# Kernel optimization log

Hardware: AMD Instinct MI355X
Metric: run time of the kernel (lower is better)

## Reference

```python
import jax, jax.numpy as jnp
import numpy as np

NUM_HEADS = 32
NUM_KV_HEADS = 8
HEAD_DIM = 128
HIDDEN = 4096
ROPE_THETA = 10000.0
RMS_EPS = 1e-6


def setup_inputs() -> dict:
    key = jax.random.key(0)
    k1, k2, k3 = jax.random.split(key, 3)
    T = 2048
    qkv_out = (NUM_HEADS + 2 * NUM_KV_HEADS) * HEAD_DIM  # 6144
    return {
        "positions": jnp.arange(T, dtype=jnp.int64),
        "hidden_states": jax.random.normal(k1, (T, HIDDEN), dtype=jnp.float32),
        "wqkv": jax.random.normal(k2, (qkv_out, HIDDEN), dtype=jnp.float32) * 0.02,
        "wo": jax.random.normal(k3, (HIDDEN, NUM_HEADS * HEAD_DIM), dtype=jnp.float32) * 0.02,
        "q_norm_w": jnp.ones((HEAD_DIM,), dtype=jnp.float32),
        "k_norm_w": jnp.ones((HEAD_DIM,), dtype=jnp.float32),
    }


def _rms_norm(x, w):
    # per-head RMSNorm over last dim, computed in fp32 (matches Dots1RMSNorm)
    xf = x.astype(jnp.float32)
    var = jnp.mean(xf * xf, axis=-1, keepdims=True)
    return (w * (xf * jax.lax.rsqrt(var + RMS_EPS))).astype(x.dtype)


def _rope(x, positions):
    # NeoX-style rotary: rotate halves. x: [T, H, D]
    half = HEAD_DIM // 2
    inv_freq = 1.0 / (ROPE_THETA ** (jnp.arange(0, half, dtype=jnp.float32) / half))
    ang = positions.astype(jnp.float32)[:, None] * inv_freq  # [T, half]
    cos = jnp.cos(ang)[:, None, :]  # [T,1,half]
    sin = jnp.sin(ang)[:, None, :]
    x1, x2 = x[..., :half], x[..., half:]
    return jnp.concatenate([x1 * cos - x2 * sin, x2 * cos + x1 * sin], axis=-1)


def reference(positions, hidden_states, wqkv, wo, q_norm_w, k_norm_w):
    T = hidden_states.shape[0]
    q_size = NUM_HEADS * HEAD_DIM
    kv_size = NUM_KV_HEADS * HEAD_DIM
    qkv = hidden_states @ wqkv.T  # [T, q_size + 2*kv_size]
    q = qkv[:, :q_size].reshape(T, NUM_HEADS, HEAD_DIM)
    k = qkv[:, q_size:q_size + kv_size].reshape(T, NUM_KV_HEADS, HEAD_DIM)
    v = qkv[:, q_size + kv_size:].reshape(T, NUM_KV_HEADS, HEAD_DIM)

    q = _rms_norm(q, q_norm_w)
    k = _rms_norm(k, k_norm_w)
    q = _rope(q, positions)
    k = _rope(k, positions)

    # GQA: expand kv heads to query heads (group of 4)
    group = NUM_HEADS // NUM_KV_HEADS
    k = jnp.repeat(k, group, axis=1)  # [T, H, D]
    v = jnp.repeat(v, group, axis=1)

    scale = HEAD_DIM ** -0.5
    scores = jnp.einsum('thd,shd->hts', q, k) * scale  # [H, T, T]
    causal = positions[:, None] >= positions[None, :]
    scores = jnp.where(causal[None, :, :], scores, jnp.finfo(scores.dtype).min)
    probs = jax.nn.softmax(scores, axis=-1)
    attn = jnp.einsum('hts,shd->thd', probs, v)  # [T, H, D]
    out = attn.reshape(T, NUM_HEADS * HEAD_DIM) @ wo.T  # [T, HIDDEN]
    return out
```

## Files before the change

### kernel.cpp

```cpp
#include <hip/hip_runtime.h>


#define T_SEQ 2048
#define HID   4096
#define NH    32
#define NKVH  8
#define HD    128
#define QKVN  6144
#define QSZ   4096
#define QKN   5120

typedef unsigned short u16;
typedef __attribute__((ext_vector_type(8))) short short8;
typedef __attribute__((ext_vector_type(4))) float floatx4;

__device__ __forceinline__ float bf2f(u16 u) {
  union { unsigned int i; float f; } c; c.i = ((unsigned int)u) << 16; return c.f;
}
__device__ __forceinline__ u16 f2bf(float f) {
  union { float f; unsigned int i; } c; c.f = f;
  unsigned int u = c.i;
  return (u16)((u + 0x7FFFu + ((u >> 16) & 1u)) >> 16);
}
__device__ __forceinline__ floatx4 mfma16(short8 a, short8 b, floatx4 c) {
  return __builtin_amdgcn_mfma_f32_16x16x32_bf16(a, b, c, 0, 0, 0);
}

#define GLD16(g, l) __builtin_amdgcn_global_load_lds( \
    (__attribute__((address_space(1))) unsigned int*)(g), \
    (__attribute__((address_space(3))) unsigned int*)(l), 16, 0, 0)

__global__ __launch_bounds__(256) void cvt3_kernel(
    const float* __restrict__ s0, const float* __restrict__ s1,
    const float* __restrict__ s2, u16* __restrict__ d0, u16* __restrict__ d1,
    u16* __restrict__ d2, int n0, int n1, int n2) {
  int total = n0 + n1 + n2;
  int stride = gridDim.x * 256;
  for (int i = blockIdx.x * 256 + threadIdx.x; i < total; i += stride) {
    const float* s; u16* d; int j = i;
    if (j < n0)           { s = s0; d = d0; }
    else if (j < n0 + n1) { j -= n0; s = s1; d = d1; }
    else                  { j -= n0 + n1; s = s2; d = d2; }
    float4 a = ((const float4*)s)[2 * j];
    float4 b = ((const float4*)s)[2 * j + 1];
    union { ushort u[8]; uint4 v; } o;
    o.u[0] = f2bf(a.x); o.u[1] = f2bf(a.y); o.u[2] = f2bf(a.z); o.u[3] = f2bf(a.w);
    o.u[4] = f2bf(b.x); o.u[5] = f2bf(b.y); o.u[6] = f2bf(b.z); o.u[7] = f2bf(b.w);
    ((uint4*)d)[j] = o.v;
  }
}

template <int MODE>
__global__ __launch_bounds__(256, 2) void gemm_bt(const u16* __restrict__ A,
    const u16* __restrict__ B, void* __restrict__ Cv, u16* __restrict__ VT,
    int mtiles, int K, int ldC) {
  __shared__ __attribute__((aligned(16))) u16 As[128 * 64];
  __shared__ __attribute__((aligned(16))) u16 Bs[128 * 64];
  const int tid = threadIdx.x;
  const int wave = tid >> 6, lane = tid & 63;
  const int lq = lane >> 4, lc = lane & 15;
  const int wm = wave >> 1, wn = wave & 1;
  const int id = ((int)blockIdx.x & 7) * ((int)gridDim.x >> 3) + ((int)blockIdx.x >> 3);
  const int by = id % mtiles, bx = id / mtiles;
  const int m0 = by * 128, n0 = bx * 128;

  floatx4 acc[4][4];
#pragma unroll
  for (int i = 0; i < 4; ++i)
#pragma unroll
    for (int j = 0; j < 4; ++j) acc[i][j] = {0.f, 0.f, 0.f, 0.f};

  int arow[4], brow[4];
#pragma unroll
  for (int i = 0; i < 4; ++i) {
    arow[i] = wm * 64 + i * 16 + lc;
    brow[i] = wn * 64 + i * 16 + lc;
  }

  const u16* asrc[4]; const u16* bsrc[4];
#pragma unroll
  for (int r = 0; r < 4; ++r) {
    int L = r * 256 + tid;
    int mm = L >> 3;
    int cc = (L & 7) ^ (mm & 7);
    asrc[r] = A + (size_t)(m0 + mm) * K + cc * 8;
    bsrc[r] = B + (size_t)(n0 + mm) * K + cc * 8;
  }

  for (int k0 = 0; k0 < K; k0 += 64) {
#pragma unroll
    for (int r = 0; r < 4; ++r) {
      GLD16(asrc[r] + k0, As + (r * 256 + wave * 64) * 8);
      GLD16(bsrc[r] + k0, Bs + (r * 256 + wave * 64) * 8);
    }
    __syncthreads();
#pragma unroll
    for (int kb = 0; kb < 2; ++kb) {
      short8 af[4], bfr[4];
#pragma unroll
      for (int mi = 0; mi < 4; ++mi)
        af[mi] = *(const short8*)&As[arow[mi] * 64 + (((kb * 4 + lq) ^ (arow[mi] & 7)) * 8)];
#pragma unroll
      for (int ni = 0; ni < 4; ++ni)
        bfr[ni] = *(const short8*)&Bs[brow[ni] * 64 + (((kb * 4 + lq) ^ (brow[ni] & 7)) * 8)];
#pragma unroll
      for (int mi = 0; mi < 4; ++mi)
#pragma unroll
        for (int ni = 0; ni < 4; ++ni)
          acc[mi][ni] = mfma16(af[mi], bfr[ni], acc[mi][ni]);
    }
    __syncthreads();
  }

  if (MODE == 1 && n0 >= 5120) {
#pragma unroll
    for (int mi = 0; mi < 4; ++mi) {
      int row = m0 + wm * 64 + mi * 16 + lq * 4;
#pragma unroll
      for (int ni = 0; ni < 4; ++ni) {
        int rel = n0 + wn * 64 + ni * 16 + lc - 5120;
        ushort4 u;
        u.x = f2bf(acc[mi][ni][0]); u.y = f2bf(acc[mi][ni][1]);
        u.z = f2bf(acc[mi][ni][2]); u.w = f2bf(acc[mi][ni][3]);
        *(ushort4*)&VT[(size_t)rel * T_SEQ + row] = u;
      }
    }
  } else {
#pragma unroll
    for (int mi = 0; mi < 4; ++mi) {
      int row = m0 + wm * 64 + mi * 16 + lq * 4;
#pragma unroll
      for (int ni = 0; ni < 4; ++ni) {
        int col = n0 + wn * 64 + ni * 16 + lc;
#pragma unroll
        for (int r = 0; r < 4; ++r) {
          if (MODE == 1)
            ((u16*)Cv)[(size_t)(row + r) * ldC + col] = f2bf(acc[mi][ni][r]);
          else
            ((float*)Cv)[(size_t)(row + r) * ldC + col] = acc[mi][ni][r];
        }
      }
    }
  }
}

__global__ __launch_bounds__(256) void norm_rope_kernel(const u16* __restrict__ qk,
    const float* __restrict__ qw, const float* __restrict__ kw,
    u16* __restrict__ Qo, u16* __restrict__ Ko) {
  const int t = blockIdx.x;
  const int w = threadIdx.x >> 6;
  const int l = threadIdx.x & 63;
  const int half = l >> 5;
  const int d0 = (l & 31) * 4;
  const int fi = d0 & 63;
  float c4[4], s4[4];
#pragma unroll
  for (int j = 0; j < 4; ++j) {
    float invf = exp2f((float)(fi + j) * -0.20762050593045158f);
    __sincosf((float)t * invf, &s4[j], &c4[j]);
  }
  const bool hi = (d0 >= 64);
  const u16* row = qk + (size_t)t * QKN;
#pragma unroll
  for (int it = 0; it < 5; ++it) {
    const int p = w * 2 + it * 8;
    const int hs = p + half;
    const bool isq = p < NH;
    const float* wptr = isq ? qw : kw;
    float4 wv = *(const float4*)(wptr + d0);
    ushort4 xv = *(const ushort4*)(row + hs * HD + d0);
    float x0 = bf2f(xv.x), x1 = bf2f(xv.y), x2 = bf2f(xv.z), x3 = bf2f(xv.w);
    float ss = x0 * x0 + x1 * x1 + x2 * x2 + x3 * x3;
#pragma unroll
    for (int m = 1; m < 32; m <<= 1) ss += __shfl_xor(ss, m);
    float rstd = rsqrtf(ss * (1.0f / HD) + 1e-6f);
    float n0 = x0 * rstd * wv.x;
    float n1 = x1 * rstd * wv.y;
    float n2 = x2 * rstd * wv.z;
    float n3 = x3 * rstd * wv.w;
    float p0 = __shfl_xor(n0, 16);
    float p1 = __shfl_xor(n1, 16);
    float p2 = __shfl_xor(n2, 16);
    float p3 = __shfl_xor(n3, 16);
    float o0, o1, o2, o3;
    if (!hi) {
      o0 = n0 * c4[0] - p0 * s4[0];
      o1 = n1 * c4[1] - p1 * s4[1];
      o2 = n2 * c4[2] - p2 * s4[2];
      o3 = n3 * c4[3] - p3 * s4[3];
    } else {
      o0 = n0 * c4[0] + p0 * s4[0];
      o1 = n1 * c4[1] + p1 * s4[1];
      o2 = n2 * c4[2] + p2 * s4[2];
      o3 = n3 * c4[3] + p3 * s4[3];
    }
    ushort4 ov;
    if (isq) {
      const float sc = 0.08838834764831845f;
      ov.x = f2bf(o0 * sc); ov.y = f2bf(o1 * sc);
      ov.z = f2bf(o2 * sc); ov.w = f2bf(o3 * sc);
      *(ushort4*)(Qo + ((size_t)hs * T_SEQ + t) * HD + d0) = ov;
    } else {
      ov.x = f2bf(o0); ov.y = f2bf(o1); ov.z = f2bf(o2); ov.w = f2bf(o3);
      *(ushort4*)(Ko + ((size_t)(hs - NH) * T_SEQ + t) * HD + d0) = ov;
    }
  }
}

__global__ __launch_bounds__(256, 2) void attn_kernel(const u16* __restrict__ Qg,
    const u16* __restrict__ Kg, const u16* __restrict__ VTg, u16* __restrict__ Og) {
  __shared__ __attribute__((aligned(16))) u16 Ks[2][8192];
  __shared__ __attribute__((aligned(16))) u16 Vs[2][8192];
  __shared__ __attribute__((aligned(16))) u16 Ps[8192];

  const int bid = blockIdx.x;
  const int h = bid & 31;
  const int qq = bid >> 5;
  const int qt = (qq < 8) ? (15 - qq) : (qq - 8);
  const int kvh = h >> 2;
  const int tid = threadIdx.x;
  const int wave = tid >> 6, lane = tid & 63;
  const int lq = lane >> 4, lc = lane & 15;

  const u16* kbase[4];
  const u16* vbase[4];
#pragma unroll
  for (int i = 0; i < 4; ++i) {
    int L = i * 256 + tid;
    int s = L >> 4, cp = L & 15;
    kbase[i] = Kg + ((size_t)kvh * T_SEQ + s) * HD + ((cp ^ (s & 15)) * 8);
    int d = L >> 3, cv = L & 7;
    vbase[i] = VTg + ((size_t)kvh * HD + d) * T_SEQ + ((cv ^ (d & 7)) * 8);
  }

  short8 qf[2][4];
#pragma unroll
  for (int mb = 0; mb < 2; ++mb)
#pragma unroll
    for (int ks = 0; ks < 4; ++ks) {
      int t = qt * 128 + wave * 32 + mb * 16 + lc;
      qf[mb][ks] = *(const short8*)&Qg[((size_t)h * T_SEQ + t) * HD + ks * 32 + lq * 8];
    }

  short8 ones;
#pragma unroll
  for (int j = 0; j < 8; ++j) ones[j] = (short)0x3F80;

  floatx4 of[2][8];
  floatx4 lacc[2];
#pragma unroll
  for (int mb = 0; mb < 2; ++mb) {
    lacc[mb] = {0.f, 0.f, 0.f, 0.f};
#pragma unroll
    for (int db = 0; db < 8; ++db) of[mb][db] = {0.f, 0.f, 0.f, 0.f};
  }

  const int ktmax = 2 * qt + 1;
  const int t0g = qt * 128 + wave * 32;
  const int wave_tmax = t0g + 31;

#pragma unroll
  for (int i = 0; i < 4; ++i) {
    GLD16(kbase[i], Ks[0] + (i * 256 + wave * 64) * 8);
    GLD16(vbase[i], Vs[0] + (i * 256 + wave * 64) * 8);
  }

  for (int kt = 0; kt <= ktmax; ++kt) {
    __syncthreads();
    if (kt + 1 <= ktmax) {
      u16* vd = Vs[(kt + 1) & 1] + (size_t)wave * 64 * 8;
      u16* kd = Ks[(kt + 1) & 1] + (size_t)wave * 64 * 8;
#pragma unroll
      for (int i = 0; i < 4; ++i) {
        GLD16(vbase[i] + (kt + 1) * 64, vd + i * 256 * 8);
        GLD16(kbase[i] + (size_t)(kt + 1) * 8192, kd + i * 256 * 8);
      }
    }
    const bool active = (kt * 64) <= wave_tmax;
    if (active) {
      floatx4 sf[2][4];
#pragma unroll
      for (int mb = 0; mb < 2; ++mb)
#pragma unroll
        for (int nb = 0; nb < 4; ++nb) sf[mb][nb] = {0.f, 0.f, 0.f, 0.f};
      const u16* kb = Ks[kt & 1];
#pragma unroll
      for (int ks = 0; ks < 4; ++ks) {
        short8 kf[4];
#pragma unroll
        for (int nb = 0; nb < 4; ++nb)
          kf[nb] = *(const short8*)&kb[(nb * 16 + lc) * 128 + ((4 * ks + lq) ^ lc) * 8];
#pragma unroll
        for (int mb = 0; mb < 2; ++mb)
#pragma unroll
          for (int nb = 0; nb < 4; ++nb)
            sf[mb][nb] = mfma16(kf[nb], qf[mb][ks], sf[mb][nb]);
      }
      const bool nm = (kt * 64 + 63) > t0g;
#pragma unroll
      for (int mb = 0; mb < 2; ++mb) {
        const int trow = wave * 32 + mb * 16 + lc;
        const int tg = qt * 128 + trow;
#pragma unroll
        for (int nb = 0; nb < 4; ++nb) {
          ushort4 u;
          float p0 = __expf(sf[mb][nb][0]);
          float p1 = __expf(sf[mb][nb][1]);
          float p2 = __expf(sf[mb][nb][2]);
          float p3 = __expf(sf[mb][nb][3]);
          if (nm) {
            int sg = kt * 64 + nb * 16 + lq * 4;
            p0 = (sg + 0 <= tg) ? p0 : 0.f;
            p1 = (sg + 1 <= tg) ? p1 : 0.f;
            p2 = (sg + 2 <= tg) ? p2 : 0.f;
            p3 = (sg + 3 <= tg) ? p3 : 0.f;
          }
          u.x = f2bf(p0); u.y = f2bf(p1); u.z = f2bf(p2); u.w = f2bf(p3);
          int c = 2 * nb + (lq >> 1);
          *(ushort4*)&Ps[trow * 64 + ((c ^ (trow & 7)) * 8) + (lq & 1) * 4] = u;
        }
      }
    }
    __syncthreads();
    if (active) {
      const u16* vb = Vs[kt & 1];
      short8 pf[2][2];
#pragma unroll
      for (int mb = 0; mb < 2; ++mb)
#pragma unroll
        for (int k2 = 0; k2 < 2; ++k2) {
          int trow = wave * 32 + mb * 16 + lc;
          pf[mb][k2] =
              *(const short8*)&Ps[trow * 64 + (((4 * k2 + lq) ^ (lc & 7)) * 8)];
        }
#pragma unroll
      for (int k2 = 0; k2 < 2; ++k2) {
#pragma unroll
        for (int db = 0; db < 8; ++db) {
          short8 vf =
              *(const short8*)&vb[(db * 16 + lc) * 64 + (((4 * k2 + lq) ^ (lc & 7)) * 8)];
          of[0][db] = mfma16(pf[0][k2], vf, of[0][db]);
          of[1][db] = mfma16(pf[1][k2], vf, of[1][db]);
        }
        lacc[0] = mfma16(pf[0][k2], ones, lacc[0]);
        lacc[1] = mfma16(pf[1][k2], ones, lacc[1]);
      }
    }
  }
#pragma unroll
  for (int mb = 0; mb < 2; ++mb)
#pragma unroll
    for (int r = 0; r < 4; ++r) {
      float inv = 1.f / lacc[mb][r];
      int tg = qt * 128 + wave * 32 + mb * 16 + lq * 4 + r;
#pragma unroll
      for (int db = 0; db < 8; ++db)
        Og[(size_t)tg * QSZ + h * HD + db * 16 + lc] = f2bf(of[mb][db][r] * inv);
    }
}

extern "C" void kernel_launch(void* const* d_in, const int* in_sizes, int n_in,
                              void* d_out, int out_size, void* d_ws, size_t ws_size,
                              hipStream_t stream) {
  (void)in_sizes; (void)n_in; (void)out_size; (void)ws_size;
  const float* hidden = (const float*)d_in[1];
  const float* wqkv   = (const float*)d_in[2];
  const float* wo     = (const float*)d_in[3];
  const float* qw     = (const float*)d_in[4];
  const float* kw     = (const float*)d_in[5];
  float* out = (float*)d_out;
  char* ws = (char*)d_ws;

  u16* h_bf    = (u16*)(ws + 0);
  u16* wq_bf   = (u16*)(ws + 16777216);
  u16* wo_bf   = (u16*)(ws + 67108864);
  u16* vT_bf   = (u16*)(ws + 100663296);
  u16* qk_bf   = (u16*)(ws + 104857600);
  u16* q_bf    = (u16*)(ws + 16777216);
  u16* k_bf    = (u16*)(ws + 33554432);
  u16* attn_bf = (u16*)(ws + 0);

  cvt3_kernel<<<4096, 256, 0, stream>>>(
      hidden, wqkv, wo, h_bf, wq_bf, wo_bf,
      T_SEQ * HID / 8, QKVN * HID / 8, HID * QSZ / 8);

  gemm_bt<1><<<768, 256, 0, stream>>>(h_bf, wq_bf, qk_bf, vT_bf,
                                      T_SEQ / 128, HID, QKN);

  norm_rope_kernel<<<T_SEQ, 256, 0, stream>>>(qk_bf, qw, kw, q_bf, k_bf);

  attn_kernel<<<512, 256, 0, stream>>>(q_bf, k_bf, vT_bf, attn_bf);

  gemm_bt<0><<<512, 256, 0, stream>>>(attn_bf, wo_bf, out, vT_bf,
                                      T_SEQ / 128, HID, QSZ);
}
```

Baseline: 484.1 us.

## Overlap wo conversion with QKV GEMM and single-buffer K in attention

The wo fp32-to-bf16 conversion moves out of the standalone convert kernel into 256 extra blocks appended to the QKV GEMM launch, so the conversion runs alongside GEMM tiles instead of before them. The attention kernel drops K double buffering: it uses one K buffer and issues the next K tile's load after the second barrier, once the QK^T reads are done. This frees LDS, possibly allowing higher occupancy, but exposes K load latency during the PV phase. The extra conversion blocks also compete with GEMM blocks for CUs and bandwidth.

```diff
diff --git a/kernel.cpp b/kernel.cpp
--- a/kernel.cpp
+++ b/kernel.cpp
@@ -30,17 +30,15 @@
     (__attribute__((address_space(1))) unsigned int*)(g), \
     (__attribute__((address_space(3))) unsigned int*)(l), 16, 0, 0)
 
-__global__ __launch_bounds__(256) void cvt3_kernel(
+__global__ __launch_bounds__(256) void cvt2_kernel(
     const float* __restrict__ s0, const float* __restrict__ s1,
-    const float* __restrict__ s2, u16* __restrict__ d0, u16* __restrict__ d1,
-    u16* __restrict__ d2, int n0, int n1, int n2) {
-  int total = n0 + n1 + n2;
+    u16* __restrict__ d0, u16* __restrict__ d1, int n0, int n1) {
+  int total = n0 + n1;
   int stride = gridDim.x * 256;
   for (int i = blockIdx.x * 256 + threadIdx.x; i < total; i += stride) {
     const float* s; u16* d; int j = i;
-    if (j < n0)           { s = s0; d = d0; }
-    else if (j < n0 + n1) { j -= n0; s = s1; d = d1; }
-    else                  { j -= n0 + n1; s = s2; d = d2; }
+    if (j < n0) { s = s0; d = d0; }
+    else        { j -= n0; s = s1; d = d1; }
     float4 a = ((const float4*)s)[2 * j];
     float4 b = ((const float4*)s)[2 * j + 1];
     union { ushort u[8]; uint4 v; } o;
@@ -53,14 +51,30 @@
 template <int MODE>
 __global__ __launch_bounds__(256, 2) void gemm_bt(const u16* __restrict__ A,
     const u16* __restrict__ B, void* __restrict__ Cv, u16* __restrict__ VT,
-    int mtiles, int K, int ldC) {
+    int mtiles, int K, int ldC,
+    const float* __restrict__ xsrc, u16* __restrict__ xdst, int xgroups,
+    int gemm_grid) {
   __shared__ __attribute__((aligned(16))) u16 As[128 * 64];
   __shared__ __attribute__((aligned(16))) u16 Bs[128 * 64];
   const int tid = threadIdx.x;
+
+  if ((int)blockIdx.x >= gemm_grid) {
+    const int nthr = ((int)gridDim.x - gemm_grid) * 256;
+    for (int i = ((int)blockIdx.x - gemm_grid) * 256 + tid; i < xgroups; i += nthr) {
+      float4 a = ((const float4*)xsrc)[2 * i];
+      float4 b = ((const float4*)xsrc)[2 * i + 1];
+      union { ushort u[8]; uint4 v; } o;
+      o.u[0] = f2bf(a.x); o.u[1] = f2bf(a.y); o.u[2] = f2bf(a.z); o.u[3] = f2bf(a.w);
+      o.u[4] = f2bf(b.x); o.u[5] = f2bf(b.y); o.u[6] = f2bf(b.z); o.u[7] = f2bf(b.w);
+      ((uint4*)xdst)[i] = o.v;
+    }
+    return;
+  }
+
   const int wave = tid >> 6, lane = tid & 63;
   const int lq = lane >> 4, lc = lane & 15;
   const int wm = wave >> 1, wn = wave & 1;
-  const int id = ((int)blockIdx.x & 7) * ((int)gridDim.x >> 3) + ((int)blockIdx.x >> 3);
+  const int id = ((int)blockIdx.x & 7) * (gemm_grid >> 3) + ((int)blockIdx.x >> 3);
   const int by = id % mtiles, bx = id / mtiles;
   const int m0 = by * 128, n0 = bx * 128;
 
@@ -209,7 +223,7 @@
 
 __global__ __launch_bounds__(256, 2) void attn_kernel(const u16* __restrict__ Qg,
     const u16* __restrict__ Kg, const u16* __restrict__ VTg, u16* __restrict__ Og) {
-  __shared__ __attribute__((aligned(16))) u16 Ks[2][8192];
+  __shared__ __attribute__((aligned(16))) u16 Ks[8192];
   __shared__ __attribute__((aligned(16))) u16 Vs[2][8192];
   __shared__ __attribute__((aligned(16))) u16 Ps[8192];
 
@@ -261,7 +275,7 @@
 
 #pragma unroll
   for (int i = 0; i < 4; ++i) {
-    GLD16(kbase[i], Ks[0] + (i * 256 + wave * 64) * 8);
+    GLD16(kbase[i], Ks + (i * 256 + wave * 64) * 8);
     GLD16(vbase[i], Vs[0] + (i * 256 + wave * 64) * 8);
   }
 
@@ -269,12 +283,9 @@
     __syncthreads();
     if (kt + 1 <= ktmax) {
       u16* vd = Vs[(kt + 1) & 1] + (size_t)wave * 64 * 8;
-      u16* kd = Ks[(kt + 1) & 1] + (size_t)wave * 64 * 8;
-#pragma unroll
-      for (int i = 0; i < 4; ++i) {
+#pragma unroll
+      for (int i = 0; i < 4; ++i)
         GLD16(vbase[i] + (kt + 1) * 64, vd + i * 256 * 8);
-        GLD16(kbase[i] + (size_t)(kt + 1) * 8192, kd + i * 256 * 8);
-      }
     }
     const bool active = (kt * 64) <= wave_tmax;
     if (active) {
@@ -283,13 +294,12 @@
       for (int mb = 0; mb < 2; ++mb)
 #pragma unroll
         for (int nb = 0; nb < 4; ++nb) sf[mb][nb] = {0.f, 0.f, 0.f, 0.f};
-      const u16* kb = Ks[kt & 1];
 #pragma unroll
       for (int ks = 0; ks < 4; ++ks) {
         short8 kf[4];
 #pragma unroll
         for (int nb = 0; nb < 4; ++nb)
-          kf[nb] = *(const short8*)&kb[(nb * 16 + lc) * 128 + ((4 * ks + lq) ^ lc) * 8];
+          kf[nb] = *(const short8*)&Ks[(nb * 16 + lc) * 128 + ((4 * ks + lq) ^ lc) * 8];
 #pragma unroll
         for (int mb = 0; mb < 2; ++mb)
 #pragma unroll
@@ -322,6 +332,12 @@
       }
     }
     __syncthreads();
+    if (kt + 1 <= ktmax) {
+      u16* kd = Ks + (size_t)wave * 64 * 8;
+#pragma unroll
+      for (int i = 0; i < 4; ++i)
+        GLD16(kbase[i] + (size_t)(kt + 1) * 8192, kd + i * 256 * 8);
+    }
     if (active) {
       const u16* vb = Vs[kt & 1];
       short8 pf[2][2];
@@ -380,17 +396,18 @@
   u16* k_bf    = (u16*)(ws + 33554432);
   u16* attn_bf = (u16*)(ws + 0);
 
-  cvt3_kernel<<<4096, 256, 0, stream>>>(
-      hidden, wqkv, wo, h_bf, wq_bf, wo_bf,
-      T_SEQ * HID / 8, QKVN * HID / 8, HID * QSZ / 8);
-
-  gemm_bt<1><<<768, 256, 0, stream>>>(h_bf, wq_bf, qk_bf, vT_bf,
-                                      T_SEQ / 128, HID, QKN);
+  cvt2_kernel<<<4096, 256, 0, stream>>>(
+      hidden, wqkv, h_bf, wq_bf, T_SEQ * HID / 8, QKVN * HID / 8);
+
+  gemm_bt<1><<<1024, 256, 0, stream>>>(h_bf, wq_bf, qk_bf, vT_bf,
+                                       T_SEQ / 128, HID, QKN,
+                                       wo, wo_bf, HID * QSZ / 8, 768);
 
   norm_rope_kernel<<<T_SEQ, 256, 0, stream>>>(qk_bf, qw, kw, q_bf, k_bf);
 
   attn_kernel<<<512, 256, 0, stream>>>(q_bf, k_bf, vT_bf, attn_bf);
 
   gemm_bt<0><<<512, 256, 0, stream>>>(attn_bf, wo_bf, out, vT_bf,
-                                      T_SEQ / 128, HID, QSZ);
-}
+                                      T_SEQ / 128, HID, QSZ,
+                                      nullptr, nullptr, 0, 512);
+}
```

Result: faster. 474.1 us (-2.1%).
